# Kernel optimization log

Hardware: AMD Instinct MI355X
Metric: run time of the kernel (lower is better)

The kernel has to match this reference:

```python
import jax, jax.numpy as jnp
import numpy as np

B = 8192
D_IN = 1024
H = 1024
N_LAYERS = 10  # 1 input layer + 9 hidden layers, then output layer H->1


def setup_inputs() -> dict:
    key = jax.random.key(0)
    ks = jax.random.split(key, 7)
    s_in = 1.0 / np.sqrt(D_IN)
    s_h = 1.0 / np.sqrt(H)
    return {
        "x": jax.random.normal(ks[0], (B, D_IN), dtype=jnp.float32),
        "W0": jax.random.normal(ks[1], (H, D_IN), dtype=jnp.float32) * s_in,
        "b0": jax.random.normal(ks[2], (H,), dtype=jnp.float32) * s_in,
        "Wh": jax.random.normal(ks[3], (N_LAYERS - 1, H, H), dtype=jnp.float32) * s_h,
        "bh": jax.random.normal(ks[4], (N_LAYERS - 1, H), dtype=jnp.float32) * s_h,
        "Wout": jax.random.normal(ks[5], (1, H), dtype=jnp.float32) * s_h,
        "bout": jax.random.normal(ks[6], (1,), dtype=jnp.float32) * s_h,
    }


def reference(x, W0, b0, Wh, bh, Wout, bout):
    # First layer: Linear(D_IN -> H) + sigmoid. torch Linear is x @ W.T + b.
    h = jax.nn.sigmoid(x @ W0.T + b0)  # [B, H]

    # Remaining num_layers-1 hidden layers, identical shape -> lax.scan over stacked weights.
    def step(h, wb):
        W, b = wb
        return jax.nn.sigmoid(h @ W.T + b), None

    h, _ = jax.lax.scan(step, h, (Wh, bh))

    # Output layer: Linear(H -> 1), no activation.
    return h @ Wout.T + bout  # [B, 1]
```

## Files before the change

### kernel.cpp

```cpp
#include <hip/hip_runtime.h>
#include <stdint.h>

typedef unsigned int u32;
typedef _Float16 f16;
typedef __attribute__((ext_vector_type(16))) float    f32x16;
typedef __attribute__((ext_vector_type(4)))  float    f32x4;
typedef __attribute__((ext_vector_type(8)))  _Float16 f16x8;
typedef __attribute__((ext_vector_type(4)))  _Float16 f16x4;

#define DIM    1024
#define NROWS  8192
#define NLAYER 10

__global__ __launch_bounds__(256) void pack_weights(const float* __restrict__ W0,
                                                    const float* __restrict__ Wh,
                                                    f16* __restrict__ Wp) {
    int g    = blockIdx.x * 4 + (threadIdx.x >> 6);
    int lane = threadIdx.x & 63;
    int l    = g >> 11;
    int c32  = (g >> 6) & 31;
    int kc   = g & 63;
    int n  = c32 * 32 + (lane & 31);
    int k  = kc * 16 + (lane >> 5) * 8;
    const float* src = (l == 0 ? W0 : Wh + (size_t)(l - 1) * DIM * DIM) + (size_t)n * DIM + k;
    float4 w0 = *(const float4*)src;
    float4 w1 = *(const float4*)(src + 4);
    f16x8 o;
    o[0] = (f16)w0.x; o[1] = (f16)w0.y; o[2] = (f16)w0.z; o[3] = (f16)w0.w;
    o[4] = (f16)w1.x; o[5] = (f16)w1.y; o[6] = (f16)w1.z; o[7] = (f16)w1.w;
    *(f16x8*)((char*)Wp + (size_t)g * 1024 + lane * 16) = o;
}

__global__ __launch_bounds__(512, 2) void mono_chain(
        const float* __restrict__ x,
        const f16* __restrict__ Wp,
        const float* __restrict__ b0,
        const float* __restrict__ bh,
        const float* __restrict__ Wout,
        const float* __restrict__ bout,
        float* __restrict__ out) {
    __shared__ char lds[2 * 65536];

    const int tid  = threadIdx.x;
    const int lane = tid & 63;
    const int wid  = tid >> 6;
    const int bid  = blockIdx.x;
    const int r0   = bid * 32;

    {
        const float* xs = x + (size_t)r0 * DIM;
        #pragma unroll
        for (int it = 0; it < 16; ++it) {
            int f = it * 2048 + tid * 4;
            float4 v = *(const float4*)(xs + f);
            f16x4 o;
            o.x = (f16)v.x; o.y = (f16)v.y; o.z = (f16)v.z; o.w = (f16)v.w;
            int r  = f >> 10;
            int kb = (f & 1023) * 2;
            *(f16x4*)(lds + r * 2048 + (kb ^ ((r & 7) << 4))) = o;
        }
    }
    __syncthreads();

    const int c0    = wid * 128;
    const int arow  = (lane & 31) * 2048;
    const int ahalf = (lane >> 5) * 16;
    const int aslot = ((lane & 31) & 7) << 4;

    int curbuf = 0;
    for (int l = 0; l < NLAYER; ++l) {
        const char* wbase = (const char*)Wp + (size_t)l * 2097152
                          + (size_t)(wid * 4) * 65536 + lane * 16;
        const char* hb = lds + curbuf * 65536;
        char*       hn = lds + (curbuf ^ 1) * 65536;

        f32x16 acc[4];
        #pragma unroll
        for (int nf = 0; nf < 4; ++nf) acc[nf] = (f32x16)(0.f);

        f16x8 bA[4], aA;
        #pragma unroll
        for (int nf = 0; nf < 4; ++nf)
            bA[nf] = *(const f16x8*)(wbase + nf * 65536);
        aA = *(const f16x8*)(hb + arow + (ahalf ^ aslot));

        #pragma unroll 2
        for (int kc = 0; kc < 64; ++kc) {
            int nk = (kc + 1) & 63;
            f16x8 bN[4], aN;
            #pragma unroll
            for (int nf = 0; nf < 4; ++nf)
                bN[nf] = *(const f16x8*)(wbase + nf * 65536 + (size_t)nk * 1024);
            aN = *(const f16x8*)(hb + arow + ((nk * 32 + ahalf) ^ aslot));

            __builtin_amdgcn_s_setprio(1);
            #pragma unroll
            for (int nf = 0; nf < 4; ++nf)
                acc[nf] = __builtin_amdgcn_mfma_f32_32x32x16_f16(bA[nf], aA, acc[nf], 0, 0, 0);
            __builtin_amdgcn_s_setprio(0);

            #pragma unroll
            for (int nf = 0; nf < 4; ++nf) bA[nf] = bN[nf];
            aA = aN;
        }

        const float* bias = l ? (bh + (size_t)(l - 1) * DIM) : b0;
        const int r  = lane & 31;
        const int rs = (r & 7) << 4;
        #pragma unroll
        for (int nf = 0; nf < 4; ++nf) {
            #pragma unroll
            for (int g2 = 0; g2 < 4; ++g2) {
                int cb = c0 + nf * 32 + g2 * 8 + 4 * (lane >> 5);
                f32x4 bv = *(const f32x4*)(bias + cb);
                f16x4 o;
                #pragma unroll
                for (int j = 0; j < 4; ++j) {
                    float z = acc[nf][g2 * 4 + j] + bv[j];
                    o[j] = (f16)(1.0f / (1.0f + __expf(-z)));
                }
                *(f16x4*)(hn + r * 2048 + ((cb * 2) ^ rs)) = o;
            }
        }
        __syncthreads();
        curbuf ^= 1;
    }

    {
        const char* hf  = lds + curbuf * 65536;
        int row = tid >> 4;
        int seg = tid & 15;
        int rs  = (row & 7) << 4;
        float s = 0.f;
        #pragma unroll
        for (int i = 0; i < 8; ++i) {
            int k0 = seg * 64 + i * 8;
            f16x8 h8 = *(const f16x8*)(hf + row * 2048 + ((k0 * 2) ^ rs));
            const float* w = Wout + k0;
            f32x4 w0 = *(const f32x4*)w;
            f32x4 w1 = *(const f32x4*)(w + 4);
            s += (float)h8[0] * w0[0] + (float)h8[1] * w0[1]
               + (float)h8[2] * w0[2] + (float)h8[3] * w0[3]
               + (float)h8[4] * w1[0] + (float)h8[5] * w1[1]
               + (float)h8[6] * w1[2] + (float)h8[7] * w1[3];
        }
        #pragma unroll
        for (int off = 8; off > 0; off >>= 1)
            s += __shfl_down(s, off, 16);
        if (seg == 0) out[r0 + row] = s + bout[0];
    }
}

extern "C" void kernel_launch(void* const* d_in, const int* in_sizes, int n_in,
                              void* d_out, int out_size, void* d_ws, size_t ws_size,
                              hipStream_t stream) {
    const float* x    = (const float*)d_in[0];
    const float* W0   = (const float*)d_in[1];
    const float* b0   = (const float*)d_in[2];
    const float* Wh   = (const float*)d_in[3];
    const float* bh   = (const float*)d_in[4];
    const float* Wout = (const float*)d_in[5];
    const float* bout = (const float*)d_in[6];
    float* out = (float*)d_out;

    f16* Wp = (f16*)d_ws;

    pack_weights<<<NLAYER * 32 * 64 / 4, 256, 0, stream>>>(W0, Wh, Wp);
    mono_chain<<<NROWS / 32, 512, 0, stream>>>(x, Wp, b0, bh, Wout, bout, out);
}
```

Before: 251.6 us.

## Use 16 waves per block with MFMA-native LDS layout and triple-buffered loads

Doubles the block to 1024 threads, so each of 16 waves computes 64 output columns (2 MFMA tiles) instead of 128, which halves per-wave register pressure and raises the number of waves available to hide latency. The activation buffer in LDS moves from a row-major XOR-swizzled layout to a chunked layout that matches the MFMA operand fragments, so each lane reads contiguous 16 bytes. The K loop is rewritten with a 3-deep rotating register prefetch of weights and activations. The risk is that only one block per CU fits (128KB LDS), and each block's weights now stream through more waves, which adds per-wave L2 traffic.

```diff
diff --git a/kernel.cpp b/kernel.cpp
--- a/kernel.cpp
+++ b/kernel.cpp
@@ -31,10 +31,10 @@
     *(f16x8*)((char*)Wp + (size_t)g * 1024 + lane * 16) = o;
 }
 
-__global__ __launch_bounds__(512, 2) void mono_chain(
+__global__ __launch_bounds__(1024, 4) void mono_chain(
         const float* __restrict__ x,
         const f16* __restrict__ Wp,
-        const float* __restrict__ b0,
+        const float* __restrict__ b0g,
         const float* __restrict__ bh,
         const float* __restrict__ Wout,
         const float* __restrict__ bout,
@@ -44,82 +44,88 @@
     const int tid  = threadIdx.x;
     const int lane = tid & 63;
     const int wid  = tid >> 6;
-    const int bid  = blockIdx.x;
-    const int r0   = bid * 32;
+    const int r0   = blockIdx.x * 32;
 
     {
         const float* xs = x + (size_t)r0 * DIM;
         #pragma unroll
-        for (int it = 0; it < 16; ++it) {
-            int f = it * 2048 + tid * 4;
+        for (int it = 0; it < 8; ++it) {
+            int f = it * 4096 + tid * 4;
             float4 v = *(const float4*)(xs + f);
             f16x4 o;
             o.x = (f16)v.x; o.y = (f16)v.y; o.z = (f16)v.z; o.w = (f16)v.w;
-            int r  = f >> 10;
-            int kb = (f & 1023) * 2;
-            *(f16x4*)(lds + r * 2048 + (kb ^ ((r & 7) << 4))) = o;
+            int r = f >> 10, k = f & 1023;
+            int addr = (k >> 4) * 1024 + (r + ((k >> 3) & 1) * 32) * 16 + (k & 7) * 2;
+            *(f16x4*)(lds + addr) = o;
         }
     }
     __syncthreads();
 
-    const int c0    = wid * 128;
-    const int arow  = (lane & 31) * 2048;
-    const int ahalf = (lane >> 5) * 16;
-    const int aslot = ((lane & 31) & 7) << 4;
-
     int curbuf = 0;
     for (int l = 0; l < NLAYER; ++l) {
-        const char* wbase = (const char*)Wp + (size_t)l * 2097152
-                          + (size_t)(wid * 4) * 65536 + lane * 16;
         const char* hb = lds + curbuf * 65536;
         char*       hn = lds + (curbuf ^ 1) * 65536;
+        const char* w0 = (const char*)Wp + (size_t)l * 2097152
+                       + (size_t)(wid * 2) * 65536 + lane * 16;
+        const char* w1 = w0 + 65536;
+        const char* hL = hb + lane * 16;
 
-        f32x16 acc[4];
+        f32x16 acc0 = (f32x16)(0.f), acc1 = (f32x16)(0.f);
+
+        f16x8 a0, c0_, a1, c1_, a2, c2_, h0, h1, h2;
+        a0 = *(const f16x8*)(w0);          c0_ = *(const f16x8*)(w1);
+        h0 = *(const f16x8*)(hL);
+        a1 = *(const f16x8*)(w0 + 1024);   c1_ = *(const f16x8*)(w1 + 1024);
+        h1 = *(const f16x8*)(hL + 1024);
+        a2 = *(const f16x8*)(w0 + 2048);   c2_ = *(const f16x8*)(w1 + 2048);
+        h2 = *(const f16x8*)(hL + 2048);
+
+#define SUBSTEP(Wa, Wb, Hh, KN)                                                   \
+        __builtin_amdgcn_s_setprio(1);                                            \
+        acc0 = __builtin_amdgcn_mfma_f32_32x32x16_f16(Wa, Hh, acc0, 0, 0, 0);     \
+        acc1 = __builtin_amdgcn_mfma_f32_32x32x16_f16(Wb, Hh, acc1, 0, 0, 0);     \
+        __builtin_amdgcn_s_setprio(0);                                            \
+        Wa = *(const f16x8*)(w0 + (size_t)(KN) * 1024);                           \
+        Wb = *(const f16x8*)(w1 + (size_t)(KN) * 1024);                           \
+        Hh = *(const f16x8*)(hL + (size_t)((KN) & 63) * 1024);
+
+        for (int t = 0; t < 21; ++t) {
+            SUBSTEP(a0, c0_, h0, 3 * t + 3)
+            SUBSTEP(a1, c1_, h1, 3 * t + 4)
+            SUBSTEP(a2, c2_, h2, 3 * t + 5)
+        }
+        acc0 = __builtin_amdgcn_mfma_f32_32x32x16_f16(a0, h0, acc0, 0, 0, 0);
+        acc1 = __builtin_amdgcn_mfma_f32_32x32x16_f16(c0_, h0, acc1, 0, 0, 0);
+#undef SUBSTEP
+
+        const float* bias = l ? (bh + (size_t)(l - 1) * DIM) : b0g;
+        const int r    = lane & 31;
+        const int hsel = lane >> 5;
         #pragma unroll
-        for (int nf = 0; nf < 4; ++nf) acc[nf] = (f32x16)(0.f);
-
-        f16x8 bA[4], aA;
-        #pragma unroll
-        for (int nf = 0; nf < 4; ++nf)
-            bA[nf] = *(const f16x8*)(wbase + nf * 65536);
-        aA = *(const f16x8*)(hb + arow + (ahalf ^ aslot));
-
-        #pragma unroll 2
-        for (int kc = 0; kc < 64; ++kc) {
-            int nk = (kc + 1) & 63;
-            f16x8 bN[4], aN;
-            #pragma unroll
-            for (int nf = 0; nf < 4; ++nf)
-                bN[nf] = *(const f16x8*)(wbase + nf * 65536 + (size_t)nk * 1024);
-            aN = *(const f16x8*)(hb + arow + ((nk * 32 + ahalf) ^ aslot));
-
-            __builtin_amdgcn_s_setprio(1);
-            #pragma unroll
-            for (int nf = 0; nf < 4; ++nf)
-                acc[nf] = __builtin_amdgcn_mfma_f32_32x32x16_f16(bA[nf], aA, acc[nf], 0, 0, 0);
-            __builtin_amdgcn_s_setprio(0);
-
-            #pragma unroll
-            for (int nf = 0; nf < 4; ++nf) bA[nf] = bN[nf];
-            aA = aN;
-        }
-
-        const float* bias = l ? (bh + (size_t)(l - 1) * DIM) : b0;
-        const int r  = lane & 31;
-        const int rs = (r & 7) << 4;
-        #pragma unroll
-        for (int nf = 0; nf < 4; ++nf) {
-            #pragma unroll
-            for (int g2 = 0; g2 < 4; ++g2) {
-                int cb = c0 + nf * 32 + g2 * 8 + 4 * (lane >> 5);
+        for (int g2 = 0; g2 < 4; ++g2) {
+            {
+                int cb = wid * 64 + g2 * 8 + 4 * hsel;
                 f32x4 bv = *(const f32x4*)(bias + cb);
                 f16x4 o;
                 #pragma unroll
                 for (int j = 0; j < 4; ++j) {
-                    float z = acc[nf][g2 * 4 + j] + bv[j];
+                    float z = acc0[g2 * 4 + j] + bv[j];
                     o[j] = (f16)(1.0f / (1.0f + __expf(-z)));
                 }
-                *(f16x4*)(hn + r * 2048 + ((cb * 2) ^ rs)) = o;
+                int chunk = wid * 4 + (g2 >> 1);
+                *(f16x4*)(hn + chunk * 1024 + (r + 32 * (g2 & 1)) * 16 + hsel * 8) = o;
+            }
+            {
+                int cb = wid * 64 + 32 + g2 * 8 + 4 * hsel;
+                f32x4 bv = *(const f32x4*)(bias + cb);
+                f16x4 o;
+                #pragma unroll
+                for (int j = 0; j < 4; ++j) {
+                    float z = acc1[g2 * 4 + j] + bv[j];
+                    o[j] = (f16)(1.0f / (1.0f + __expf(-z)));
+                }
+                int chunk = wid * 4 + 2 + (g2 >> 1);
+                *(f16x4*)(hn + chunk * 1024 + (r + 32 * (g2 & 1)) * 16 + hsel * 8) = o;
             }
         }
         __syncthreads();
@@ -127,15 +133,15 @@
     }
 
     {
-        const char* hf  = lds + curbuf * 65536;
-        int row = tid >> 4;
-        int seg = tid & 15;
-        int rs  = (row & 7) << 4;
+        const char* hf = lds + curbuf * 65536;
+        int row = tid >> 5;
+        int seg = tid & 31;
         float s = 0.f;
         #pragma unroll
-        for (int i = 0; i < 8; ++i) {
-            int k0 = seg * 64 + i * 8;
-            f16x8 h8 = *(const f16x8*)(hf + row * 2048 + ((k0 * 2) ^ rs));
+        for (int i = 0; i < 4; ++i) {
+            int k0 = seg * 32 + i * 8;
+            f16x8 h8 = *(const f16x8*)(hf + (k0 >> 4) * 1024
+                                          + (row + 32 * ((k0 >> 3) & 1)) * 16);
             const float* w = Wout + k0;
             f32x4 w0 = *(const f32x4*)w;
             f32x4 w1 = *(const f32x4*)(w + 4);
@@ -145,8 +151,8 @@
                + (float)h8[6] * w1[2] + (float)h8[7] * w1[3];
         }
         #pragma unroll
-        for (int off = 8; off > 0; off >>= 1)
-            s += __shfl_down(s, off, 16);
+        for (int off = 16; off > 0; off >>= 1)
+            s += __shfl_down(s, off, 32);
         if (seg == 0) out[r0 + row] = s + bout[0];
     }
 }
@@ -166,5 +172,5 @@
     f16* Wp = (f16*)d_ws;
 
     pack_weights<<<NLAYER * 32 * 64 / 4, 256, 0, stream>>>(W0, Wh, Wp);
-    mono_chain<<<NROWS / 32, 512, 0, stream>>>(x, Wp, b0, bh, Wout, bout, out);
+    mono_chain<<<NROWS / 32, 1024, 0, stream>>>(x, Wp, b0, bh, Wout, bout, out);
 }
```

After: 242.6 us. -3.6%, faster.

## Use 64-row blocks of 16 waves with 2x2 MFMA tiles and single-buffer LDS

Applied to the files above, without the earlier changes.

Each block now processes 64 rows with 1024 threads. Each wave computes a 2x2 grid of 32x32 MFMA tiles, so every weight and activation fragment is reused twice, which halves global weight traffic per row compared with the 1x4 tiling. Activations are stored in an MFMA-fragment-ordered LDS layout instead of the XOR-swizzled row layout. One 128KB buffer is updated in place, guarded by an extra barrier before the epilogue. The cost is fewer blocks (128 instead of 256) on the chip and an added barrier per layer.

```diff
diff --git a/kernel.cpp b/kernel.cpp
--- a/kernel.cpp
+++ b/kernel.cpp
@@ -31,112 +31,124 @@
     *(f16x8*)((char*)Wp + (size_t)g * 1024 + lane * 16) = o;
 }
 
-__global__ __launch_bounds__(512, 2) void mono_chain(
+__global__ __launch_bounds__(1024, 4) void mono_chain(
         const float* __restrict__ x,
         const f16* __restrict__ Wp,
-        const float* __restrict__ b0,
+        const float* __restrict__ b0g,
         const float* __restrict__ bh,
         const float* __restrict__ Wout,
         const float* __restrict__ bout,
         float* __restrict__ out) {
-    __shared__ char lds[2 * 65536];
+    __shared__ char lds[131072];
 
     const int tid  = threadIdx.x;
     const int lane = tid & 63;
     const int wid  = tid >> 6;
-    const int bid  = blockIdx.x;
-    const int r0   = bid * 32;
+    const int r0   = blockIdx.x * 64;
 
     {
-        const float* xs = x + (size_t)r0 * DIM;
+        const int rg = lane >> 5, rr = lane & 31;
+        const float* src = x + (size_t)(r0 + lane) * DIM + wid * 64;
         #pragma unroll
-        for (int it = 0; it < 16; ++it) {
-            int f = it * 2048 + tid * 4;
-            float4 v = *(const float4*)(xs + f);
+        for (int i = 0; i < 16; ++i) {
+            float4 v = *(const float4*)(src + i * 4);
             f16x4 o;
             o.x = (f16)v.x; o.y = (f16)v.y; o.z = (f16)v.z; o.w = (f16)v.w;
-            int r  = f >> 10;
-            int kb = (f & 1023) * 2;
-            *(f16x4*)(lds + r * 2048 + (kb ^ ((r & 7) << 4))) = o;
+            int kc    = wid * 4 + (i >> 2);
+            int khalf = (i >> 1) & 1;
+            *(f16x4*)(lds + ((kc * 2 + rg) << 10) + (rr + (khalf << 5)) * 16 + (i & 1) * 8) = o;
         }
     }
     __syncthreads();
 
-    const int c0    = wid * 128;
-    const int arow  = (lane & 31) * 2048;
-    const int ahalf = (lane >> 5) * 16;
-    const int aslot = ((lane & 31) & 7) << 4;
+    const char* hL = lds + lane * 16;
 
-    int curbuf = 0;
     for (int l = 0; l < NLAYER; ++l) {
-        const char* wbase = (const char*)Wp + (size_t)l * 2097152
-                          + (size_t)(wid * 4) * 65536 + lane * 16;
-        const char* hb = lds + curbuf * 65536;
-        char*       hn = lds + (curbuf ^ 1) * 65536;
+        const char* w0 = (const char*)Wp + (size_t)l * 2097152
+                       + (size_t)wid * 131072 + lane * 16;
+        const char* w1 = w0 + 65536;
 
-        f32x16 acc[4];
-        #pragma unroll
-        for (int nf = 0; nf < 4; ++nf) acc[nf] = (f32x16)(0.f);
+        f32x16 acc00 = (f32x16)(0.f), acc01 = (f32x16)(0.f);
+        f32x16 acc10 = (f32x16)(0.f), acc11 = (f32x16)(0.f);
 
-        f16x8 bA[4], aA;
-        #pragma unroll
-        for (int nf = 0; nf < 4; ++nf)
-            bA[nf] = *(const f16x8*)(wbase + nf * 65536);
-        aA = *(const f16x8*)(hb + arow + (ahalf ^ aslot));
+        f16x8 wA0, wB0, wA1, wB1, hA0, hB0, hA1, hB1;
+        wA0 = *(const f16x8*)(w0);
+        wB0 = *(const f16x8*)(w1);
+        hA0 = *(const f16x8*)(hL);
+        hB0 = *(const f16x8*)(hL + 1024);
+        wA1 = *(const f16x8*)(w0 + 1024);
+        wB1 = *(const f16x8*)(w1 + 1024);
+        hA1 = *(const f16x8*)(hL + 2048);
+        hB1 = *(const f16x8*)(hL + 3072);
 
-        #pragma unroll 2
-        for (int kc = 0; kc < 64; ++kc) {
-            int nk = (kc + 1) & 63;
-            f16x8 bN[4], aN;
-            #pragma unroll
-            for (int nf = 0; nf < 4; ++nf)
-                bN[nf] = *(const f16x8*)(wbase + nf * 65536 + (size_t)nk * 1024);
-            aN = *(const f16x8*)(hb + arow + ((nk * 32 + ahalf) ^ aslot));
+#define STEP(WA, WB, HA, HB, KN)                                                 \
+        __builtin_amdgcn_s_setprio(1);                                           \
+        acc00 = __builtin_amdgcn_mfma_f32_32x32x16_f16(WA, HA, acc00, 0, 0, 0);  \
+        acc10 = __builtin_amdgcn_mfma_f32_32x32x16_f16(WB, HA, acc10, 0, 0, 0);  \
+        acc01 = __builtin_amdgcn_mfma_f32_32x32x16_f16(WA, HB, acc01, 0, 0, 0);  \
+        acc11 = __builtin_amdgcn_mfma_f32_32x32x16_f16(WB, HB, acc11, 0, 0, 0);  \
+        __builtin_amdgcn_s_setprio(0);                                           \
+        WA = *(const f16x8*)(w0 + (size_t)(KN) * 1024);                          \
+        WB = *(const f16x8*)(w1 + (size_t)(KN) * 1024);                          \
+        HA = *(const f16x8*)(hL + (size_t)(KN) * 2048);                          \
+        HB = *(const f16x8*)(hL + (size_t)(KN) * 2048 + 1024);
 
-            __builtin_amdgcn_s_setprio(1);
-            #pragma unroll
-            for (int nf = 0; nf < 4; ++nf)
-                acc[nf] = __builtin_amdgcn_mfma_f32_32x32x16_f16(bA[nf], aA, acc[nf], 0, 0, 0);
-            __builtin_amdgcn_s_setprio(0);
+        for (int t = 0; t < 31; ++t) {
+            STEP(wA0, wB0, hA0, hB0, 2 * t + 2)
+            STEP(wA1, wB1, hA1, hB1, 2 * t + 3)
+        }
+#undef STEP
+        acc00 = __builtin_amdgcn_mfma_f32_32x32x16_f16(wA0, hA0, acc00, 0, 0, 0);
+        acc10 = __builtin_amdgcn_mfma_f32_32x32x16_f16(wB0, hA0, acc10, 0, 0, 0);
+        acc01 = __builtin_amdgcn_mfma_f32_32x32x16_f16(wA0, hB0, acc01, 0, 0, 0);
+        acc11 = __builtin_amdgcn_mfma_f32_32x32x16_f16(wB0, hB0, acc11, 0, 0, 0);
+        acc00 = __builtin_amdgcn_mfma_f32_32x32x16_f16(wA1, hA1, acc00, 0, 0, 0);
+        acc10 = __builtin_amdgcn_mfma_f32_32x32x16_f16(wB1, hA1, acc10, 0, 0, 0);
+        acc01 = __builtin_amdgcn_mfma_f32_32x32x16_f16(wA1, hB1, acc01, 0, 0, 0);
+        acc11 = __builtin_amdgcn_mfma_f32_32x32x16_f16(wB1, hB1, acc11, 0, 0, 0);
 
-            #pragma unroll
-            for (int nf = 0; nf < 4; ++nf) bA[nf] = bN[nf];
-            aA = aN;
+        __syncthreads();
+
+        const float* bias = l ? (bh + (size_t)(l - 1) * DIM) : b0g;
+        const int rD   = lane & 31;
+        const int hsel = lane >> 5;
+#define EPI(ACC, CG, RGP)                                                        \
+        {                                                                        \
+            _Pragma("unroll")                                                    \
+            for (int g2 = 0; g2 < 4; ++g2) {                                     \
+                int c = (wid * 2 + (CG)) * 32 + g2 * 8 + 4 * hsel;               \
+                f32x4 bv = *(const f32x4*)(bias + c);                            \
+                f16x4 o;                                                         \
+                _Pragma("unroll")                                                \
+                for (int j = 0; j < 4; ++j) {                                    \
+                    float z = ACC[g2 * 4 + j] + bv[j];                           \
+                    o[j] = (f16)(1.0f / (1.0f + __expf(-z)));                    \
+                }                                                                \
+                int kc2 = (wid * 2 + (CG)) * 2 + (g2 >> 1);                      \
+                *(f16x4*)(lds + ((kc2 * 2 + (RGP)) << 10)                        \
+                              + (rD + ((g2 & 1) << 5)) * 16 + hsel * 8) = o;     \
+            }                                                                    \
         }
-
-        const float* bias = l ? (bh + (size_t)(l - 1) * DIM) : b0;
-        const int r  = lane & 31;
-        const int rs = (r & 7) << 4;
-        #pragma unroll
-        for (int nf = 0; nf < 4; ++nf) {
-            #pragma unroll
-            for (int g2 = 0; g2 < 4; ++g2) {
-                int cb = c0 + nf * 32 + g2 * 8 + 4 * (lane >> 5);
-                f32x4 bv = *(const f32x4*)(bias + cb);
-                f16x4 o;
-                #pragma unroll
-                for (int j = 0; j < 4; ++j) {
-                    float z = acc[nf][g2 * 4 + j] + bv[j];
-                    o[j] = (f16)(1.0f / (1.0f + __expf(-z)));
-                }
-                *(f16x4*)(hn + r * 2048 + ((cb * 2) ^ rs)) = o;
-            }
-        }
+        EPI(acc00, 0, 0)
+        EPI(acc01, 0, 1)
+        EPI(acc10, 1, 0)
+        EPI(acc11, 1, 1)
+#undef EPI
         __syncthreads();
-        curbuf ^= 1;
     }
 
     {
-        const char* hf  = lds + curbuf * 65536;
         int row = tid >> 4;
         int seg = tid & 15;
-        int rs  = (row & 7) << 4;
+        int rg = row >> 5, rr = row & 31;
         float s = 0.f;
         #pragma unroll
         for (int i = 0; i < 8; ++i) {
-            int k0 = seg * 64 + i * 8;
-            f16x8 h8 = *(const f16x8*)(hf + row * 2048 + ((k0 * 2) ^ rs));
-            const float* w = Wout + k0;
+            int k  = seg * 64 + i * 8;
+            int kc = k >> 4;
+            f16x8 h8 = *(const f16x8*)(lds + ((kc * 2 + rg) << 10)
+                                           + (rr + ((i & 1) << 5)) * 16);
+            const float* w = Wout + k;
             f32x4 w0 = *(const f32x4*)w;
             f32x4 w1 = *(const f32x4*)(w + 4);
             s += (float)h8[0] * w0[0] + (float)h8[1] * w0[1]
@@ -166,5 +178,5 @@
     f16* Wp = (f16*)d_ws;
 
     pack_weights<<<NLAYER * 32 * 64 / 4, 256, 0, stream>>>(W0, Wh, Wp);
-    mono_chain<<<NROWS / 32, 512, 0, stream>>>(x, Wp, b0, bh, Wout, bout, out);
+    mono_chain<<<NROWS / 64, 1024, 0, stream>>>(x, Wp, b0, bh, Wout, bout, out);
 }
```

Result: slower. 340.4 us (+35.3%).
